# Optimization experiments

Measured on AMD Instinct MI355X. Metric: run time of the kernel, lower is better.

Reference implementation:

```python
import jax, jax.numpy as jnp
import numpy as np

B, S, D, H = 1, 4096, 1024, 16
HD = D // H  # head_dim = 64
NEG = -1e9

def setup_inputs() -> dict:
    key = jax.random.key(0)
    ks = jax.random.split(key, 5)
    scale = 1.0 / np.sqrt(D)
    x = jax.random.normal(ks[0], (B, S, D), dtype=jnp.float32)
    Wq = jax.random.normal(ks[1], (D, D), dtype=jnp.float32) * scale
    Wk = jax.random.normal(ks[2], (D, D), dtype=jnp.float32) * scale
    Wv = jax.random.normal(ks[3], (D, D), dtype=jnp.float32) * scale
    Wo = jax.random.normal(ks[4], (D, D), dtype=jnp.float32) * scale
    mask = jnp.tril(jnp.ones((S, S), dtype=bool))[None, None]  # [1,1,S,S] causal
    return {"x": x, "mask": mask, "Wq": Wq, "Wk": Wk, "Wv": Wv, "Wo": Wo}

def reference(x, mask, Wq, Wk, Wv, Wo):
    # Linear projections (bias=False). nn.Linear computes x @ W.T; weights here
    # are stored as [out, in] so we use x @ W.T for faithfulness.
    q = x @ Wq.T  # [B,S,D]
    k = x @ Wk.T
    v = x @ Wv.T
    def split_heads(t):
        return t.reshape(B, S, H, HD).transpose(0, 2, 1, 3)  # [B,H,S,HD]
    q, k, v = split_heads(q), split_heads(k), split_heads(v)
    scores = jnp.einsum("bhqd,bhkd->bhqk", q, k) / jnp.sqrt(jnp.float32(HD))
    scores = jnp.where(mask, scores, NEG)
    attn = jax.nn.softmax(scores, axis=-1)  # dropout p=0.0 -> identity
    out = jnp.einsum("bhqk,bhkd->bhqd", attn, v)  # [B,H,S,HD]
    out = out.transpose(0, 2, 1, 3).reshape(B, S, D)
    return out @ Wo.T
```

## Files before the change

kernel.cpp:

```cpp
#include <hip/hip_runtime.h>
#include <hip/hip_bf16.h>


typedef __bf16 bf16x8 __attribute__((ext_vector_type(8)));
typedef __bf16 bf16x4 __attribute__((ext_vector_type(4)));
typedef float f32x4 __attribute__((ext_vector_type(4)));
typedef short s16x4 __attribute__((ext_vector_type(4)));

#define GAS __attribute__((address_space(1)))
#define LAS __attribute__((address_space(3)))

__device__ __forceinline__ void async_copy16(const void* g, void* l) {
  __builtin_amdgcn_global_load_lds((const GAS unsigned int*)g,
                                   (LAS unsigned int*)l, 16, 0, 0);
}

__device__ __forceinline__ f32x4 mfma_k16(bf16x4 a, bf16x4 b, f32x4 c) {
  union { bf16x4 h; s16x4 s; } ua, ub;
  ua.h = a; ub.h = b;
  return __builtin_amdgcn_mfma_f32_16x16x16bf16_1k(ua.s, ub.s, c, 0, 0, 0);
}

__global__ __launch_bounds__(256) void cvt_all(const float* __restrict__ x,
                                               const float* __restrict__ Wq,
                                               const float* __restrict__ Wk,
                                               const float* __restrict__ Wv,
                                               const float* __restrict__ Wo,
                                               __bf16* __restrict__ xb,
                                               __bf16* __restrict__ Wc,
                                               __bf16* __restrict__ Wob) {
  int b = blockIdx.x;
  const float* src;
  __bf16* dst;
  if (b < 4096)      { src = x  + (b       ) * 1024; dst = xb  + (long)b * 1024; }
  else if (b < 5120) { src = Wq + (b - 4096) * 1024; dst = Wc  + (long)(b - 4096) * 1024; }
  else if (b < 6144) { src = Wk + (b - 5120) * 1024; dst = Wc  + (1l << 20) + (long)(b - 5120) * 1024; }
  else if (b < 7168) { src = Wv + (b - 6144) * 1024; dst = Wc  + (2l << 20) + (long)(b - 6144) * 1024; }
  else               { src = Wo + (b - 7168) * 1024; dst = Wob + (long)(b - 7168) * 1024; }
  int i = threadIdx.x * 4;
  float4 f = *(const float4*)(src + i);
  bf16x4 o;
  o[0] = (__bf16)f.x; o[1] = (__bf16)f.y; o[2] = (__bf16)f.z; o[3] = (__bf16)f.w;
  *(bf16x4*)(dst + i) = o;
}

__global__ __launch_bounds__(256) void gemm_qkv(const __bf16* __restrict__ A,
                                                const __bf16* __restrict__ B,
                                                __bf16* __restrict__ Qb,
                                                __bf16* __restrict__ Kf,
                                                __bf16* __restrict__ Vf) {
  const int K = 1024;
  __shared__ __bf16 As[128 * 32];
  __shared__ __bf16 Bs[128 * 32];
  const int tid = threadIdx.x;
  const int lane = tid & 63, wv = tid >> 6;
  const int l15 = lane & 15, quad = lane >> 4;
  const int wm = wv >> 1, wn = wv & 1;
  const int mbase = blockIdx.y * 128, nbase = blockIdx.x * 128;
  const bool swp = (nbase < 2048);

  f32x4 acc[4][4] = {};

  for (int k0 = 0; k0 < K; k0 += 32) {
    __syncthreads();
#pragma unroll
    for (int q = 0; q < 2; ++q) {
      int i = q * 256 + tid;
      int row = i >> 2, kg = i & 3;
      const __bf16* ga = A + (long)(mbase + row) * K + k0 + kg * 8;
      const __bf16* gb = B + (long)(nbase + row) * K + k0 + kg * 8;
      char* la = (char*)As + (q * 256 + wv * 64) * 16;
      char* lb = (char*)Bs + (q * 256 + wv * 64) * 16;
      async_copy16(ga, la);
      async_copy16(gb, lb);
    }
    __syncthreads();
    bf16x8 af[4], bfr[4];
#pragma unroll
    for (int i = 0; i < 4; ++i)
      af[i] = *(const bf16x8*)&As[(wm * 64 + i * 16 + l15) * 32 + quad * 8];
#pragma unroll
    for (int j = 0; j < 4; ++j)
      bfr[j] = *(const bf16x8*)&Bs[(wn * 64 + j * 16 + l15) * 32 + quad * 8];
    if (swp) {
#pragma unroll
      for (int i = 0; i < 4; ++i)
#pragma unroll
        for (int j = 0; j < 4; ++j)
          acc[i][j] = __builtin_amdgcn_mfma_f32_16x16x32_bf16(bfr[j], af[i], acc[i][j], 0, 0, 0);
    } else {
#pragma unroll
      for (int i = 0; i < 4; ++i)
#pragma unroll
        for (int j = 0; j < 4; ++j)
          acc[i][j] = __builtin_amdgcn_mfma_f32_16x16x32_bf16(af[i], bfr[j], acc[i][j], 0, 0, 0);
    }
  }

  if (nbase < 1024) {
    const float QS = 0.18033688011112043f;
#pragma unroll
    for (int i = 0; i < 4; ++i) {
      int row = mbase + wm * 64 + i * 16 + l15;
#pragma unroll
      for (int j = 0; j < 4; ++j) {
        int cb = nbase + wn * 64 + j * 16 + quad * 4;
        union { __bf16 b[4]; uint2 u; } pk;
#pragma unroll
        for (int r = 0; r < 4; ++r) pk.b[r] = (__bf16)(acc[i][j][r] * QS);
        *(uint2*)(Qb + (long)row * 1024 + cb) = pk.u;
      }
    }
  } else if (nbase < 2048) {
#pragma unroll
    for (int i = 0; i < 4; ++i)
#pragma unroll
      for (int j = 0; j < 4; ++j) {
        int d0 = nbase - 1024 + wn * 64 + j * 16 + quad * 4;
        int h = d0 >> 6, dd = d0 & 63;
        int kk = dd >> 5, qf = (dd >> 3) & 3, e0 = dd & 7;
        int kt = mbase + wm * 64 + i * 16 + l15;
        int tile = kt >> 6;
        long off = ((long)(h * 64 + tile) * 8 + i * 2 + kk) * 512 + (qf * 16 + l15) * 8 + e0;
        union { __bf16 b[4]; uint2 u; } pk;
#pragma unroll
        for (int r = 0; r < 4; ++r) pk.b[r] = (__bf16)acc[i][j][r];
        *(uint2*)(Kf + off) = pk.u;
      }
  } else {
#pragma unroll
    for (int i = 0; i < 4; ++i)
#pragma unroll
      for (int j = 0; j < 4; ++j) {
        int col = nbase - 2048 + wn * 64 + j * 16 + l15;
        int h = col >> 6, dd = col & 63;
        int jd = dd >> 4, lv = dd & 15;
        int kt0 = mbase + wm * 64 + i * 16 + quad * 4;
        int tile = kt0 >> 6, w6 = kt0 & 63;
        int jp = w6 >> 5, bit4 = (w6 >> 4) & 1, qv = (w6 >> 2) & 3;
        long off = ((long)(h * 64 + tile) * 8 + jd * 2 + jp) * 512 + (qv * 16 + lv) * 8 + bit4 * 4;
        union { __bf16 b[4]; uint2 u; } pk;
#pragma unroll
        for (int r = 0; r < 4; ++r) pk.b[r] = (__bf16)acc[i][j][r];
        *(uint2*)(Vf + off) = pk.u;
      }
  }
}

__global__ __launch_bounds__(256) void gemm_wo(const __bf16* __restrict__ A,
                                               const __bf16* __restrict__ B,
                                               float* __restrict__ C) {
  const int K = 1024, N = 1024;
  __shared__ __bf16 As[128 * 32];
  __shared__ __bf16 Bs[64 * 32];
  const int tid = threadIdx.x;
  const int lane = tid & 63, wv = tid >> 6;
  const int l15 = lane & 15, quad = lane >> 4;
  const int wm = wv >> 1, wn = wv & 1;
  const int mbase = blockIdx.y * 128, nbase = blockIdx.x * 64;

  f32x4 acc[4][2] = {};

  for (int k0 = 0; k0 < K; k0 += 32) {
    __syncthreads();
#pragma unroll
    for (int q = 0; q < 2; ++q) {
      int i = q * 256 + tid;
      int row = i >> 2, kg = i & 3;
      const __bf16* ga = A + (long)(mbase + row) * K + k0 + kg * 8;
      char* la = (char*)As + (q * 256 + wv * 64) * 16;
      async_copy16(ga, la);
    }
    {
      int row = tid >> 2, kg = tid & 3;
      const __bf16* gb = B + (long)(nbase + row) * K + k0 + kg * 8;
      char* lb = (char*)Bs + (wv * 64) * 16;
      async_copy16(gb, lb);
    }
    __syncthreads();
    bf16x8 af[4], bfr[2];
#pragma unroll
    for (int i = 0; i < 4; ++i)
      af[i] = *(const bf16x8*)&As[(wm * 64 + i * 16 + l15) * 32 + quad * 8];
#pragma unroll
    for (int j = 0; j < 2; ++j)
      bfr[j] = *(const bf16x8*)&Bs[(wn * 32 + j * 16 + l15) * 32 + quad * 8];
#pragma unroll
    for (int i = 0; i < 4; ++i)
#pragma unroll
      for (int j = 0; j < 2; ++j)
        acc[i][j] = __builtin_amdgcn_mfma_f32_16x16x32_bf16(bfr[j], af[i], acc[i][j], 0, 0, 0);
  }
#pragma unroll
  for (int i = 0; i < 4; ++i) {
    int row = mbase + wm * 64 + i * 16 + l15;
#pragma unroll
    for (int j = 0; j < 2; ++j) {
      int cb = nbase + wn * 32 + j * 16 + quad * 4;
      *(f32x4*)(C + (long)row * N + cb) = acc[i][j];
    }
  }
}

__global__ __launch_bounds__(512, 2) void flash_attn(const __bf16* __restrict__ Qb,
                                                     const __bf16* __restrict__ Kf,
                                                     const __bf16* __restrict__ Vf,
                                                     __bf16* __restrict__ AO) {
  __shared__ float Ms[2][3][64][34];
  const int tid = threadIdx.x;
  const int lane = tid & 63, l15 = lane & 15, quad = lane >> 4;
  const int w = tid >> 6;
  const int pr = w >> 2, qtr = w & 3;
  const int b = blockIdx.x;
  const int h = (b & 7) + 8 * ((b >> 3) & 1);
  const int rest = b >> 4;
  const int P = rest * 2 + pr;
  const int hoff = h * 64;

  const __bf16* Kh = Kf + (long)h * 64 * 4096;
  const __bf16* Vh = Vf + (long)h * 64 * 4096;

  for (int pass = 0; pass < 2; ++pass) {
    const int T = pass ? (127 - P) : P;
    bf16x8 qf[2][2];
#pragma unroll
    for (int g = 0; g < 2; ++g) {
      const int qrow = T * 32 + g * 16 + l15;
      qf[g][0] = *(const bf16x8*)(Qb + (long)qrow * 1024 + hoff + quad * 8);
      qf[g][1] = *(const bf16x8*)(Qb + (long)qrow * 1024 + hoff + 32 + quad * 8);
    }

    const int nkt = (T >> 1) + 1;
    const int kt0 = (nkt * qtr) >> 2;
    const int kt1 = (nkt * (qtr + 1)) >> 2;
    f32x4 o_acc[2][4] = {};
    float l_acc[2] = {0.0f, 0.0f};

    bf16x8 kc[8];
    if (kt0 < kt1) {
      const __bf16* Kt = Kh + (long)kt0 * 4096;
#pragma unroll
      for (int f = 0; f < 8; ++f)
        kc[f] = *(const bf16x8*)(Kt + f * 512 + lane * 8);
    }

    for (int kt = kt0; kt < kt1; ++kt) {
      const __bf16* Vt = Vh + (long)kt * 4096;

      bf16x8 va[8];
#pragma unroll
      for (int f = 0; f < 8; ++f)
        va[f] = *(const bf16x8*)(Vt + f * 512 + lane * 8);

      f32x4 st[2][4] = {};
#pragma unroll
      for (int g = 0; g < 2; ++g)
#pragma unroll
        for (int j = 0; j < 4; ++j) {
          st[g][j] = __builtin_amdgcn_mfma_f32_16x16x32_bf16(kc[j * 2 + 0], qf[g][0], st[g][j], 0, 0, 0);
          st[g][j] = __builtin_amdgcn_mfma_f32_16x16x32_bf16(kc[j * 2 + 1], qf[g][1], st[g][j], 0, 0, 0);
        }

      if (kt + 1 < kt1) {
        const __bf16* Kt = Kh + (long)(kt + 1) * 4096;
#pragma unroll
        for (int f = 0; f < 8; ++f)
          kc[f] = *(const bf16x8*)(Kt + f * 512 + lane * 8);
      }

      if (kt == nkt - 1) {
#pragma unroll
        for (int g = 0; g < 2; ++g) {
          const int dq = (T & 1) * 32 + g * 16 + l15;
#pragma unroll
          for (int j = 0; j < 4; ++j)
#pragma unroll
            for (int r = 0; r < 4; ++r)
              if (j * 16 + quad * 4 + r > dq) st[g][j][r] = -3.0e38f;
        }
      }

      bf16x4 pb[2][4];
#pragma unroll
      for (int g = 0; g < 2; ++g) {
        float ps = 0.0f;
#pragma unroll
        for (int j = 0; j < 4; ++j) {
          f32x4 pj;
#pragma unroll
          for (int r = 0; r < 4; ++r) pj[r] = __builtin_amdgcn_exp2f(st[g][j][r]);
          ps += (pj[0] + pj[1]) + (pj[2] + pj[3]);
          bf16x4 bb;
#pragma unroll
          for (int r = 0; r < 4; ++r) bb[r] = (__bf16)pj[r];
          pb[g][j] = bb;
        }
        l_acc[g] += ps;
      }

#pragma unroll
      for (int g = 0; g < 2; ++g)
#pragma unroll
        for (int j = 0; j < 4; ++j) {
          bf16x4 pbj = pb[g][j];
#pragma unroll
          for (int jd = 0; jd < 4; ++jd) {
            bf16x8 v8 = va[jd * 2 + (j >> 1)];
            bf16x4 a4 = (j & 1) ? __builtin_shufflevector(v8, v8, 4, 5, 6, 7)
                                : __builtin_shufflevector(v8, v8, 0, 1, 2, 3);
            o_acc[g][jd] = mfma_k16(a4, pbj, o_acc[g][jd]);
          }
        }
    }

    if (qtr) {
#pragma unroll
      for (int g = 0; g < 2; ++g) {
#pragma unroll
        for (int jd = 0; jd < 4; ++jd)
#pragma unroll
          for (int r = 0; r < 4; ++r)
            Ms[pr][qtr - 1][lane][g * 16 + jd * 4 + r] = o_acc[g][jd][r];
        Ms[pr][qtr - 1][lane][32 + g] = l_acc[g];
      }
    }
    __syncthreads();
    if (!qtr) {
#pragma unroll
      for (int g = 0; g < 2; ++g) {
#pragma unroll
        for (int s = 0; s < 3; ++s)
#pragma unroll
          for (int jd = 0; jd < 4; ++jd)
#pragma unroll
            for (int r = 0; r < 4; ++r)
              o_acc[g][jd][r] += Ms[pr][s][lane][g * 16 + jd * 4 + r];
        float la = l_acc[g] + Ms[pr][0][lane][32 + g] + Ms[pr][1][lane][32 + g] + Ms[pr][2][lane][32 + g];
        la += __shfl_xor(la, 16);
        la += __shfl_xor(la, 32);
        const float inv = 1.0f / la;
        const int qrow = T * 32 + g * 16 + l15;
#pragma unroll
        for (int jd = 0; jd < 4; ++jd) {
          bf16x4 ob;
#pragma unroll
          for (int r = 0; r < 4; ++r) ob[r] = (__bf16)(o_acc[g][jd][r] * inv);
          *(bf16x4*)(AO + (long)qrow * 1024 + hoff + jd * 16 + quad * 4) = ob;
        }
      }
    }
    __syncthreads();
  }
}

extern "C" void kernel_launch(void* const* d_in, const int* in_sizes, int n_in,
                              void* d_out, int out_size, void* d_ws, size_t ws_size,
                              hipStream_t stream) {
  const float* x  = (const float*)d_in[0];
  const float* Wq = (const float*)d_in[2];
  const float* Wk = (const float*)d_in[3];
  const float* Wv = (const float*)d_in[4];
  const float* Wo = (const float*)d_in[5];
  float* out = (float*)d_out;

  char* ws = (char*)d_ws;
  __bf16* xb  = (__bf16*)ws;
  __bf16* Wc  = (__bf16*)(ws + (8u << 20));
  __bf16* Wob = (__bf16*)(ws + (14u << 20));
  __bf16* Qb  = (__bf16*)(ws + (16u << 20));
  __bf16* Kfr = (__bf16*)(ws + (24u << 20));
  __bf16* Vfr = (__bf16*)(ws + (32u << 20));
  __bf16* AO  = (__bf16*)(ws + (40u << 20));

  cvt_all<<<8192, 256, 0, stream>>>(x, Wq, Wk, Wv, Wo, xb, Wc, Wob);

  dim3 g1(3072 / 128, 4096 / 128);
  gemm_qkv<<<g1, 256, 0, stream>>>(xb, Wc, Qb, Kfr, Vfr);

  flash_attn<<<512, 512, 0, stream>>>(Qb, Kfr, Vfr, AO);

  dim3 g2(1024 / 64, 4096 / 128);
  gemm_wo<<<g2, 256, 0, stream>>>(AO, Wob, out);
}
```

Measured before the change: 241.3 us.

## Remap GEMM tiles per XCD and split attention keys across two waves

Both GEMMs switch to a 1D grid and remap block IDs so that the blocks landing on each XCD share a narrow band of N columns, which should improve L2 reuse of the weight tiles. The flash attention kernel now puts four query-tile pairs per block, each split across 2 waves instead of 4, and launches half as many blocks. The cross-wave reduction through LDS becomes a single partner merge. This trades less intra-tile key parallelism for less reduction traffic and fewer blocks, which risks longer per-wave work on long causal rows.

```diff
diff --git a/kernel.cpp b/kernel.cpp
--- a/kernel.cpp
+++ b/kernel.cpp
@@ -56,7 +56,11 @@
   const int lane = tid & 63, wv = tid >> 6;
   const int l15 = lane & 15, quad = lane >> 4;
   const int wm = wv >> 1, wn = wv & 1;
-  const int mbase = blockIdx.y * 128, nbase = blockIdx.x * 128;
+  const int bb = blockIdx.x;
+  const int xcd = bb & 7, q = bb >> 3;
+  const int nb = xcd * 3 + (q % 3);
+  const int mb = q / 3;
+  const int mbase = mb * 128, nbase = nb * 128;
   const bool swp = (nbase < 2048);
 
   f32x4 acc[4][4] = {};
@@ -64,13 +68,13 @@
   for (int k0 = 0; k0 < K; k0 += 32) {
     __syncthreads();
 #pragma unroll
-    for (int q = 0; q < 2; ++q) {
-      int i = q * 256 + tid;
+    for (int p = 0; p < 2; ++p) {
+      int i = p * 256 + tid;
       int row = i >> 2, kg = i & 3;
       const __bf16* ga = A + (long)(mbase + row) * K + k0 + kg * 8;
       const __bf16* gb = B + (long)(nbase + row) * K + k0 + kg * 8;
-      char* la = (char*)As + (q * 256 + wv * 64) * 16;
-      char* lb = (char*)Bs + (q * 256 + wv * 64) * 16;
+      char* la = (char*)As + (p * 256 + wv * 64) * 16;
+      char* lb = (char*)Bs + (p * 256 + wv * 64) * 16;
       async_copy16(ga, la);
       async_copy16(gb, lb);
     }
@@ -157,18 +161,22 @@
   const int lane = tid & 63, wv = tid >> 6;
   const int l15 = lane & 15, quad = lane >> 4;
   const int wm = wv >> 1, wn = wv & 1;
-  const int mbase = blockIdx.y * 128, nbase = blockIdx.x * 64;
+  const int bb = blockIdx.x;
+  const int xcd = bb & 7, q = bb >> 3;
+  const int nb = xcd * 2 + (q & 1);
+  const int mb = q >> 1;
+  const int mbase = mb * 128, nbase = nb * 64;
 
   f32x4 acc[4][2] = {};
 
   for (int k0 = 0; k0 < K; k0 += 32) {
     __syncthreads();
 #pragma unroll
-    for (int q = 0; q < 2; ++q) {
-      int i = q * 256 + tid;
+    for (int p = 0; p < 2; ++p) {
+      int i = p * 256 + tid;
       int row = i >> 2, kg = i & 3;
       const __bf16* ga = A + (long)(mbase + row) * K + k0 + kg * 8;
-      char* la = (char*)As + (q * 256 + wv * 64) * 16;
+      char* la = (char*)As + (p * 256 + wv * 64) * 16;
       async_copy16(ga, la);
     }
     {
@@ -206,15 +214,15 @@
                                                      const __bf16* __restrict__ Kf,
                                                      const __bf16* __restrict__ Vf,
                                                      __bf16* __restrict__ AO) {
-  __shared__ float Ms[2][3][64][34];
+  __shared__ float Ms[4][64][35];
   const int tid = threadIdx.x;
   const int lane = tid & 63, l15 = lane & 15, quad = lane >> 4;
   const int w = tid >> 6;
-  const int pr = w >> 2, qtr = w & 3;
+  const int pr = w >> 1, half = w & 1;
   const int b = blockIdx.x;
   const int h = (b & 7) + 8 * ((b >> 3) & 1);
   const int rest = b >> 4;
-  const int P = rest * 2 + pr;
+  const int P = rest * 4 + pr;
   const int hoff = h * 64;
 
   const __bf16* Kh = Kf + (long)h * 64 * 4096;
@@ -231,8 +239,8 @@
     }
 
     const int nkt = (T >> 1) + 1;
-    const int kt0 = (nkt * qtr) >> 2;
-    const int kt1 = (nkt * (qtr + 1)) >> 2;
+    const int kt0 = half ? (nkt >> 1) : 0;
+    const int kt1 = half ? nkt : (nkt >> 1);
     f32x4 o_acc[2][4] = {};
     float l_acc[2] = {0.0f, 0.0f};
 
@@ -290,10 +298,10 @@
 #pragma unroll
           for (int r = 0; r < 4; ++r) pj[r] = __builtin_amdgcn_exp2f(st[g][j][r]);
           ps += (pj[0] + pj[1]) + (pj[2] + pj[3]);
-          bf16x4 bb;
-#pragma unroll
-          for (int r = 0; r < 4; ++r) bb[r] = (__bf16)pj[r];
-          pb[g][j] = bb;
+          bf16x4 bb16;
+#pragma unroll
+          for (int r = 0; r < 4; ++r) bb16[r] = (__bf16)pj[r];
+          pb[g][j] = bb16;
         }
         l_acc[g] += ps;
       }
@@ -313,29 +321,27 @@
         }
     }
 
-    if (qtr) {
+    if (half) {
 #pragma unroll
       for (int g = 0; g < 2; ++g) {
 #pragma unroll
         for (int jd = 0; jd < 4; ++jd)
 #pragma unroll
           for (int r = 0; r < 4; ++r)
-            Ms[pr][qtr - 1][lane][g * 16 + jd * 4 + r] = o_acc[g][jd][r];
-        Ms[pr][qtr - 1][lane][32 + g] = l_acc[g];
-      }
-    }
-    __syncthreads();
-    if (!qtr) {
+            Ms[pr][lane][g * 16 + jd * 4 + r] = o_acc[g][jd][r];
+        Ms[pr][lane][32 + g] = l_acc[g];
+      }
+    }
+    __syncthreads();
+    if (!half) {
 #pragma unroll
       for (int g = 0; g < 2; ++g) {
 #pragma unroll
-        for (int s = 0; s < 3; ++s)
-#pragma unroll
-          for (int jd = 0; jd < 4; ++jd)
-#pragma unroll
-            for (int r = 0; r < 4; ++r)
-              o_acc[g][jd][r] += Ms[pr][s][lane][g * 16 + jd * 4 + r];
-        float la = l_acc[g] + Ms[pr][0][lane][32 + g] + Ms[pr][1][lane][32 + g] + Ms[pr][2][lane][32 + g];
+        for (int jd = 0; jd < 4; ++jd)
+#pragma unroll
+          for (int r = 0; r < 4; ++r)
+            o_acc[g][jd][r] += Ms[pr][lane][g * 16 + jd * 4 + r];
+        float la = l_acc[g] + Ms[pr][lane][32 + g];
         la += __shfl_xor(la, 16);
         la += __shfl_xor(la, 32);
         const float inv = 1.0f / la;
@@ -374,11 +380,9 @@
 
   cvt_all<<<8192, 256, 0, stream>>>(x, Wq, Wk, Wv, Wo, xb, Wc, Wob);
 
-  dim3 g1(3072 / 128, 4096 / 128);
-  gemm_qkv<<<g1, 256, 0, stream>>>(xb, Wc, Qb, Kfr, Vfr);
-
-  flash_attn<<<512, 512, 0, stream>>>(Qb, Kfr, Vfr, AO);
-
-  dim3 g2(1024 / 64, 4096 / 128);
-  gemm_wo<<<g2, 256, 0, stream>>>(AO, Wob, out);
-}
+  gemm_qkv<<<768, 256, 0, stream>>>(xb, Wc, Qb, Kfr, Vfr);
+
+  flash_attn<<<256, 512, 0, stream>>>(Qb, Kfr, Vfr, AO);
+
+  gemm_wo<<<512, 256, 0, stream>>>(AO, Wob, out);
+}
```

After: 232.8 us. 1.04x faster.
